# Kernel optimization log

Measured on AMD Instinct MI355X. Metric: run time of the kernel, lower is better.

## Reference

```python
import jax, jax.numpy as jnp
import numpy as np

ALPHA = 1.0      # focal_alpha
GAMMA = 2.0      # focal_gamma
MARGIN = 0.3     # triplet_margin
T = 3.0          # kd_temperature
FW, TW, KW = 1.0, 0.5, 1.0  # focal/triplet/kd weights
NEG_INF_FILL = 1000000.0


def setup_inputs() -> dict:
    key = jax.random.key(0)
    k1, k2, k3, k4 = jax.random.split(key, 4)
    B, D, C = 4096, 512, 2
    return {
        "logits": jax.random.normal(k1, (B, C), jnp.float32),
        "features": jax.random.normal(k2, (B, D), jnp.float32),
        "hard_labels": jax.random.randint(k3, (B,), 0, 2),
        "soft_labels": jax.random.uniform(k4, (B, C), jnp.float32),
    }


def _pairwise_dist(x):
    # torch.cdist(x, x, p=2): [B, B] euclidean distances, safe sqrt (grad-safe at 0)
    sq = jnp.sum(x * x, axis=1)
    d2 = jnp.maximum(sq[:, None] + sq[None, :] - 2.0 * (x @ x.T), 0.0)
    safe = jnp.where(d2 > 0, d2, 1.0)
    return jnp.where(d2 > 0, jnp.sqrt(safe), 0.0)


def reference(logits, features, hard_labels, soft_labels):
    B = logits.shape[0]
    # ---- focal loss (integer-label branch) ----
    logp = jax.nn.log_softmax(logits, axis=-1)
    ce = -jnp.take_along_axis(logp, hard_labels[:, None], axis=1)[:, 0]
    pt = jnp.exp(-ce)
    focal = jnp.mean(ALPHA * (1.0 - pt) ** GAMMA * ce)

    # ---- triplet loss: batch-hard mining, vectorized over rows ----
    d = _pairwise_dist(features)                      # [B, B]
    same = hard_labels[:, None] == hard_labels[None, :]
    eye = jnp.eye(B, dtype=bool)
    mpos = (same & ~eye).astype(d.dtype)              # positives, diag zeroed
    mneg = (~same).astype(d.dtype)                    # negatives
    posd = d * mpos
    valid = (jnp.sum(posd, axis=1) > 0).astype(d.dtype)
    hardest_pos = jnp.max(posd, axis=1)
    hardest_neg = jnp.min(d * mneg + (1.0 - mneg) * NEG_INF_FILL, axis=1)
    per_row = jax.nn.relu(hardest_pos - hardest_neg + MARGIN)
    n_valid = jnp.sum(valid)
    triplet = jnp.where(n_valid > 0,
                        jnp.sum(per_row * valid) / jnp.maximum(n_valid, 1.0),
                        0.0)

    # ---- KD loss: KLDiv(batchmean) * T^2 ----
    student_log = jax.nn.log_softmax(logits / T, axis=-1)
    teacher = jax.nn.softmax(jnp.log(soft_labels + 1e-8) / T, axis=-1)
    kd = jnp.sum(teacher * (jnp.log(teacher) - student_log)) / B * (T ** 2)

    total = FW * focal + TW * triplet + KW * kd
    return total, focal, triplet, kd
```

## Files before the change

### kernel.cpp

```cpp
#include <hip/hip_runtime.h>
#include <hip/hip_bf16.h>

#define B_ROWS 4096
#define D_FEAT 512

typedef short s16x8 __attribute__((ext_vector_type(8)));
typedef float f32x4 __attribute__((ext_vector_type(4)));

#define GLOAD_LDS16(gsrc, ldst)                                                        \
    __builtin_amdgcn_global_load_lds(                                                  \
        (const __attribute__((address_space(1))) void*)(gsrc),                         \
        (__attribute__((address_space(3))) void*)(ldst), 16, 0, 0)

__device__ inline float waveReduceSum(float v) {
#pragma unroll
    for (int off = 32; off > 0; off >>= 1) v += __shfl_xor(v, off);
    return v;
}

__global__ __launch_bounds__(256) void prep_kernel(const float* __restrict__ feat,
                                                   const float* __restrict__ logits,
                                                   const int* __restrict__ labels,
                                                   const float* __restrict__ soft,
                                                   short* __restrict__ featbf,
                                                   float* __restrict__ sqn,
                                                   unsigned* __restrict__ posmax,
                                                   float* __restrict__ negminf,
                                                   float* __restrict__ fpart,
                                                   float* __restrict__ kpart) {
    const int bid = blockIdx.x, tid = threadIdx.x;
    const int wave = tid >> 6, lane = tid & 63;
    const int row = bid * 4 + wave;

    const float* p = feat + (size_t)row * D_FEAT + lane * 8;
    float4 a = *(const float4*)p;
    float4 b = *(const float4*)(p + 4);
    float vals[8] = {a.x, a.y, a.z, a.w, b.x, b.y, b.z, b.w};
    short outv[8];
    float s = 0.f;
#pragma unroll
    for (int j = 0; j < 8; ++j) {
        __hip_bfloat16 h = __float2bfloat16(vals[j]);
        outv[j] = *(short*)&h;
        float xb = __bfloat162float(h);
        s = fmaf(xb, xb, s);
    }
    *(s16x8*)(featbf + (size_t)row * D_FEAT + lane * 8) = *(s16x8*)outv;
    s = waveReduceSum(s);
    if (lane == 0) sqn[row] = s;

    if (tid < 4) posmax[bid * 4 + tid] = 0u;
    else if (tid < 8) negminf[bid * 4 + tid - 4] = 1e12f;

    if (bid < 16) {
        int i = bid * 256 + tid;
        float l0 = logits[2 * i], l1 = logits[2 * i + 1];

        float m = fmaxf(l0, l1);
        float lse = m + logf(expf(l0 - m) + expf(l1 - m));
        float lp = (labels[i] ? l1 : l0) - lse;
        float ce = -lp;
        float pt = expf(lp);
        float om = 1.f - pt;
        float focal = om * om * ce;

        const float Tinv = 1.f / 3.f;
        float s0 = l0 * Tinv, s1 = l1 * Tinv;
        float ms = fmaxf(s0, s1);
        float lses = ms + logf(expf(s0 - ms) + expf(s1 - ms));
        float sl0 = s0 - lses, sl1 = s1 - lses;
        float t0 = logf(soft[2 * i] + 1e-8f) * Tinv;
        float t1 = logf(soft[2 * i + 1] + 1e-8f) * Tinv;
        float mt = fmaxf(t0, t1);
        float lset = mt + logf(expf(t0 - mt) + expf(t1 - mt));
        float tl0 = t0 - lset, tl1 = t1 - lset;
        float p0 = expf(tl0), p1 = expf(tl1);
        float kd = p0 * (tl0 - sl0) + p1 * (tl1 - sl1);

        float fs = waveReduceSum(focal);
        float ks = waveReduceSum(kd);
        __shared__ float sf[4], sk[4];
        if (lane == 0) { sf[wave] = fs; sk[wave] = ks; }
        __syncthreads();
        if (tid == 0) {
            fpart[bid] = sf[0] + sf[1] + sf[2] + sf[3];
            kpart[bid] = sk[0] + sk[1] + sk[2] + sk[3];
        }
    }
}

__global__ __launch_bounds__(512) void pairwise_256_kernel(const short* __restrict__ featbf,
                                                           const float* __restrict__ sqn,
                                                           const int* __restrict__ labels,
                                                           unsigned* __restrict__ posmax,
                                                           unsigned* __restrict__ negmin) {
    __shared__ short As0[256 * 64], As1[256 * 64];
    __shared__ short Bs0[256 * 64], Bs1[256 * 64];
    const int tid = threadIdx.x;
    const int bfl = blockIdx.x;
    const int xcd = bfl & 7, loc = bfl >> 3;
    const int ib = (xcd & 3) * 4 + (loc & 3);
    const int jb = (xcd >> 1 & 2) * 4 + (loc >> 2);
    const int wid = tid >> 6, lane = tid & 63;
    const int wr = wid >> 2, wc = wid & 3;
    const int lo = lane & 15, hi = lane >> 4;

    const short* Asrc[4];
    const short* Bsrc[4];
    int dstoff[4];
#pragma unroll
    for (int q = 0; q < 4; ++q) {
        int row = q * 64 + wid * 8 + (lane >> 3);
        int c = (lane & 7) ^ (row & 7);
        Asrc[q] = featbf + (size_t)(ib * 256 + row) * D_FEAT + c * 8;
        Bsrc[q] = featbf + (size_t)(jb * 256 + row) * D_FEAT + c * 8;
        dstoff[q] = (q * 64 + wid * 8) * 64;
    }

    int aoff[2][8], boff[2][4];
#pragma unroll
    for (int ks = 0; ks < 2; ++ks) {
#pragma unroll
        for (int m = 0; m < 8; ++m) {
            int ar = wr * 128 + m * 16 + lo;
            aoff[ks][m] = ar * 64 + ((ks * 4 + hi) ^ (ar & 7)) * 8;
        }
#pragma unroll
        for (int n = 0; n < 4; ++n) {
            int bc = wc * 64 + n * 16 + lo;
            boff[ks][n] = bc * 64 + ((ks * 4 + hi) ^ (bc & 7)) * 8;
        }
    }

    f32x4 acc[8][4];
#pragma unroll
    for (int m = 0; m < 8; ++m)
#pragma unroll
        for (int n = 0; n < 4; ++n)
            acc[m][n] = (f32x4){0.f, 0.f, 0.f, 0.f};

#define STAGE_TILE(Adst, Bdst, kkv)                                                    \
    {                                                                                  \
        _Pragma("unroll") for (int q = 0; q < 4; ++q) {                                \
            GLOAD_LDS16(Asrc[q] + (kkv) * 64, (Adst) + dstoff[q]);                     \
            GLOAD_LDS16(Bsrc[q] + (kkv) * 64, (Bdst) + dstoff[q]);                     \
        }                                                                              \
    }

#define COMPUTE_TILE(Abuf, Bbuf)                                                       \
    {                                                                                  \
        _Pragma("unroll") for (int ks = 0; ks < 2; ++ks) {                             \
            s16x8 af[8], bfr[4];                                                       \
            _Pragma("unroll") for (int m = 0; m < 8; ++m)                              \
                af[m] = *(const s16x8*)((Abuf) + aoff[ks][m]);                         \
            _Pragma("unroll") for (int n = 0; n < 4; ++n)                              \
                bfr[n] = *(const s16x8*)((Bbuf) + boff[ks][n]);                        \
            _Pragma("unroll") for (int m = 0; m < 8; ++m)                              \
                _Pragma("unroll") for (int n = 0; n < 4; ++n)                          \
                    acc[m][n] = __builtin_amdgcn_mfma_f32_16x16x32_bf16(               \
                        af[m], bfr[n], acc[m][n], 0, 0, 0);                            \
        }                                                                              \
    }

    short *Aa = As0, *Ab = As1, *Ba = Bs0, *Bb = Bs1;
    STAGE_TILE(Aa, Ba, 0);
    asm volatile("s_waitcnt vmcnt(0)" ::: "memory");
    __builtin_amdgcn_s_barrier();
    __builtin_amdgcn_sched_barrier(0);

    for (int kk = 0; kk < D_FEAT / 64 - 1; ++kk) {
        STAGE_TILE(Ab, Bb, kk + 1);
        COMPUTE_TILE(Aa, Ba);
        asm volatile("s_waitcnt vmcnt(0)" ::: "memory");
        __builtin_amdgcn_s_barrier();
        __builtin_amdgcn_sched_barrier(0);
        short* t;
        t = Aa; Aa = Ab; Ab = t;
        t = Ba; Ba = Bb; Bb = t;
    }
    COMPUTE_TILE(Aa, Ba);

#undef STAGE_TILE
#undef COMPUTE_TILE

    int coln[4], labc[4];
    float sqc[4];
#pragma unroll
    for (int n = 0; n < 4; ++n) {
        coln[n] = jb * 256 + wc * 64 + n * 16 + lo;
        labc[n] = labels[coln[n]];
        sqc[n] = sqn[coln[n]];
    }
    __syncthreads();
    float (*redp)[5] = (float(*)[5])As0;
    float (*redn)[5] = ((float(*)[5])As0) + 256;

#pragma unroll
    for (int m = 0; m < 8; ++m) {
#pragma unroll
        for (int r = 0; r < 4; ++r) {
            int row_loc = wr * 128 + m * 16 + hi * 4 + r;
            int row_g = ib * 256 + row_loc;
            int labr = labels[row_g];
            float sqr = sqn[row_g];
            float pm = 0.f, nm = 1e12f;
#pragma unroll
            for (int n = 0; n < 4; ++n) {
                float d2 = fmaxf(sqr + fmaf(-2.f, acc[m][n][r], sqc[n]), 0.f);
                bool same = (labr == labc[n]);
                if (same) {
                    if (row_g != coln[n]) pm = fmaxf(pm, d2);
                } else {
                    nm = fminf(nm, d2);
                }
            }
#pragma unroll
            for (int off = 1; off < 16; off <<= 1) {
                pm = fmaxf(pm, __shfl_xor(pm, off));
                nm = fminf(nm, __shfl_xor(nm, off));
            }
            if (lo == 0) {
                redp[row_loc][wc] = pm;
                redn[row_loc][wc] = nm;
            }
        }
    }
    __syncthreads();
    if (tid < 256) {
        float p = fmaxf(fmaxf(redp[tid][0], redp[tid][1]),
                        fmaxf(redp[tid][2], redp[tid][3]));
        atomicMax(&posmax[ib * 256 + tid], __float_as_uint(p));
    } else {
        int row = tid - 256;
        float nn = fminf(fminf(redn[row][0], redn[row][1]),
                         fminf(redn[row][2], redn[row][3]));
        atomicMin(&negmin[ib * 256 + row], __float_as_uint(nn));
    }
}

__global__ __launch_bounds__(256) void finalize_kernel(const unsigned* __restrict__ posmax,
                                                       const unsigned* __restrict__ negmin,
                                                       const float* __restrict__ fpart,
                                                       const float* __restrict__ kpart,
                                                       float* __restrict__ out) {
    int tid = threadIdx.x;
    float sum_pr = 0.f, sum_v = 0.f;
    for (int i = tid; i < B_ROWS; i += 256) {
        float p2 = __uint_as_float(posmax[i]);
        float n2 = __uint_as_float(negmin[i]);
        float v = (p2 > 0.f) ? 1.f : 0.f;
        sum_pr += fmaxf(sqrtf(p2) - sqrtf(n2) + 0.3f, 0.f) * v;
        sum_v += v;
    }
    sum_pr = waveReduceSum(sum_pr);
    sum_v = waveReduceSum(sum_v);
    __shared__ float sp[4], sv[4];
    int wave = tid >> 6, lane = tid & 63;
    if (lane == 0) { sp[wave] = sum_pr; sv[wave] = sum_v; }
    __syncthreads();
    if (tid == 0) {
        float spr = sp[0] + sp[1] + sp[2] + sp[3];
        float svv = sv[0] + sv[1] + sv[2] + sv[3];
        float fsum = 0.f, ksum = 0.f;
        for (int b = 0; b < 16; ++b) { fsum += fpart[b]; ksum += kpart[b]; }
        float focal = fsum / 4096.f;
        float kd = ksum / 4096.f * 9.f;
        float triplet = (svv > 0.f) ? spr / fmaxf(svv, 1.f) : 0.f;
        float total = focal + 0.5f * triplet + kd;
        out[0] = total;
        out[1] = focal;
        out[2] = triplet;
        out[3] = kd;
    }
}

extern "C" void kernel_launch(void* const* d_in, const int* in_sizes, int n_in,
                              void* d_out, int out_size, void* d_ws, size_t ws_size,
                              hipStream_t stream) {
    const float* logits = (const float*)d_in[0];
    const float* feat   = (const float*)d_in[1];
    const int*   labels = (const int*)d_in[2];
    const float* soft   = (const float*)d_in[3];

    char* ws = (char*)d_ws;
    unsigned* posmax = (unsigned*)ws;
    unsigned* negmin = (unsigned*)(ws + 16384);
    float*    sqn    = (float*)(ws + 32768);
    float*    fpart  = (float*)(ws + 49152);
    float*    kpart  = (float*)(ws + 49152 + 256);
    short*    featbf = (short*)(ws + 65536);

    prep_kernel<<<1024, 256, 0, stream>>>(feat, logits, labels, soft, featbf, sqn,
                                          posmax, (float*)negmin, fpart, kpart);
    pairwise_256_kernel<<<256, 512, 0, stream>>>(featbf, sqn, labels, posmax, negmin);
    finalize_kernel<<<1, 256, 0, stream>>>(posmax, negmin, fpart, kpart,
                                           (float*)d_out);
}
```

Baseline: 46.03 us.

## Split pairwise GEMM K-loop into eight interleaved load/compute phases

Restructures the bf16 MFMA main loop of the pairwise-distance kernel into four phases per K tile (two M halves times two K sub-steps). Each phase issues part of the next tile's global-to-LDS loads, waits with fine-grained vmcnt counts and uses s_setprio around its MFMA block. LDS is re-laid out as 32-element K halves with a new XOR swizzle. The goal is to overlap memory traffic with matrix math instead of waiting on a full vmcnt(0) barrier every tile. In exchange it adds twice as many barriers per tile and depends on getting the hand-counted vmcnt values exactly right.

```diff
diff --git a/kernel.cpp b/kernel.cpp
--- a/kernel.cpp
+++ b/kernel.cpp
@@ -89,7 +89,7 @@
     }
 }
 
-__global__ __launch_bounds__(512) void pairwise_256_kernel(const short* __restrict__ featbf,
+__global__ __launch_bounds__(512) void pairwise_8ph_kernel(const short* __restrict__ featbf,
                                                            const float* __restrict__ sqn,
                                                            const int* __restrict__ labels,
                                                            unsigned* __restrict__ posmax,
@@ -100,36 +100,37 @@
     const int bfl = blockIdx.x;
     const int xcd = bfl & 7, loc = bfl >> 3;
     const int ib = (xcd & 3) * 4 + (loc & 3);
-    const int jb = (xcd >> 1 & 2) * 4 + (loc >> 2);
+    const int jb = ((xcd >> 1) & 2) * 4 + (loc >> 2);
     const int wid = tid >> 6, lane = tid & 63;
     const int wr = wid >> 2, wc = wid & 3;
     const int lo = lane & 15, hi = lane >> 4;
 
-    const short* Asrc[4];
-    const short* Bsrc[4];
-    int dstoff[4];
-#pragma unroll
-    for (int q = 0; q < 4; ++q) {
-        int row = q * 64 + wid * 8 + (lane >> 3);
-        int c = (lane & 7) ^ (row & 7);
-        Asrc[q] = featbf + (size_t)(ib * 256 + row) * D_FEAT + c * 8;
-        Bsrc[q] = featbf + (size_t)(jb * 256 + row) * D_FEAT + c * 8;
-        dstoff[q] = (q * 64 + wid * 8) * 64;
-    }
-
-    int aoff[2][8], boff[2][4];
-#pragma unroll
-    for (int ks = 0; ks < 2; ++ks) {
-#pragma unroll
-        for (int m = 0; m < 8; ++m) {
-            int ar = wr * 128 + m * 16 + lo;
-            aoff[ks][m] = ar * 64 + ((ks * 4 + hi) ^ (ar & 7)) * 8;
-        }
-#pragma unroll
-        for (int n = 0; n < 4; ++n) {
-            int bc = wc * 64 + n * 16 + lo;
-            boff[ks][n] = bc * 64 + ((ks * 4 + hi) ^ (bc & 7)) * 8;
-        }
+    const int rbA0 = (wid < 4) ? wid * 16 : 64 + wid * 16;
+    const int rbB0 = wid * 16;
+    const int rA0 = rbA0 + (lane >> 2), rA1 = rA0 + 64;
+    const int rB0 = rbB0 + (lane >> 2), rB1 = rB0 + 128;
+    const int cA0 = (lane & 3) ^ ((rA0 >> 1) & 3), cA1 = (lane & 3) ^ ((rA1 >> 1) & 3);
+    const int cB0 = (lane & 3) ^ ((rB0 >> 1) & 3), cB1 = (lane & 3) ^ ((rB1 >> 1) & 3);
+    const short* gA0 = featbf + (size_t)(ib * 256 + rA0) * D_FEAT + cA0 * 8;
+    const short* gA1 = featbf + (size_t)(ib * 256 + rA1) * D_FEAT + cA1 * 8;
+    const short* gB0 = featbf + (size_t)(jb * 256 + rB0) * D_FEAT + cB0 * 8;
+    const short* gB1 = featbf + (size_t)(jb * 256 + rB1) * D_FEAT + cB1 * 8;
+    const int dA0 = rbA0 * 32, dA1 = (rbA0 + 64) * 32;
+    const int dB0 = rbB0 * 32, dB1 = (rbB0 + 128) * 32;
+
+#define ISSUE(gptr, buf, dstbase, ksv, ktv)                                            \
+    GLOAD_LDS16((gptr) + (ktv) * 64 + (ksv) * 32, (buf) + (ksv) * 8192 + (dstbase))
+
+    int aoffs[8], boffs[4];
+#pragma unroll
+    for (int m = 0; m < 8; ++m) {
+        int r = wr * 128 + m * 16 + lo;
+        aoffs[m] = r * 32 + ((hi ^ ((r >> 1) & 3)) * 8);
+    }
+#pragma unroll
+    for (int n = 0; n < 4; ++n) {
+        int r = wc * 64 + n * 16 + lo;
+        boffs[n] = r * 32 + ((hi ^ ((r >> 1) & 3)) * 8);
     }
 
     f32x4 acc[8][4];
@@ -139,49 +140,77 @@
         for (int n = 0; n < 4; ++n)
             acc[m][n] = (f32x4){0.f, 0.f, 0.f, 0.f};
 
-#define STAGE_TILE(Adst, Bdst, kkv)                                                    \
+#define PHASE(mh, ksv, DO_BFR, ISSUES, VMCNT)                                          \
     {                                                                                  \
-        _Pragma("unroll") for (int q = 0; q < 4; ++q) {                                \
-            GLOAD_LDS16(Asrc[q] + (kkv) * 64, (Adst) + dstoff[q]);                     \
-            GLOAD_LDS16(Bsrc[q] + (kkv) * 64, (Bdst) + dstoff[q]);                     \
+        if (DO_BFR) {                                                                  \
+            _Pragma("unroll") for (int n = 0; n < 4; ++n)                              \
+                bfr[n] = *(const s16x8*)(Bcur + (ksv) * 8192 + boffs[n]);              \
         }                                                                              \
-    }
-
-#define COMPUTE_TILE(Abuf, Bbuf)                                                       \
-    {                                                                                  \
-        _Pragma("unroll") for (int ks = 0; ks < 2; ++ks) {                             \
-            s16x8 af[8], bfr[4];                                                       \
-            _Pragma("unroll") for (int m = 0; m < 8; ++m)                              \
-                af[m] = *(const s16x8*)((Abuf) + aoff[ks][m]);                         \
+        s16x8 af[4];                                                                   \
+        _Pragma("unroll") for (int mi = 0; mi < 4; ++mi)                               \
+            af[mi] = *(const s16x8*)(Acur + (ksv) * 8192 + aoffs[(mh) * 4 + mi]);      \
+        ISSUES;                                                                        \
+        __builtin_amdgcn_s_barrier();                                                  \
+        __builtin_amdgcn_sched_barrier(0);                                             \
+        __builtin_amdgcn_s_setprio(1);                                                 \
+        _Pragma("unroll") for (int mi = 0; mi < 4; ++mi)                               \
             _Pragma("unroll") for (int n = 0; n < 4; ++n)                              \
-                bfr[n] = *(const s16x8*)((Bbuf) + boff[ks][n]);                        \
-            _Pragma("unroll") for (int m = 0; m < 8; ++m)                              \
-                _Pragma("unroll") for (int n = 0; n < 4; ++n)                          \
-                    acc[m][n] = __builtin_amdgcn_mfma_f32_16x16x32_bf16(               \
-                        af[m], bfr[n], acc[m][n], 0, 0, 0);                            \
-        }                                                                              \
-    }
-
-    short *Aa = As0, *Ab = As1, *Ba = Bs0, *Bb = Bs1;
-    STAGE_TILE(Aa, Ba, 0);
-    asm volatile("s_waitcnt vmcnt(0)" ::: "memory");
+                acc[(mh) * 4 + mi][n] = __builtin_amdgcn_mfma_f32_16x16x32_bf16(       \
+                    af[mi], bfr[n], acc[(mh) * 4 + mi][n], 0, 0, 0);                   \
+        __builtin_amdgcn_s_setprio(0);                                                 \
+        VMCNT;                                                                         \
+        __builtin_amdgcn_s_barrier();                                                  \
+        __builtin_amdgcn_sched_barrier(0);                                             \
+    }
+
+#define VM(n) asm volatile("s_waitcnt vmcnt(" #n ")" ::: "memory")
+
+    const short* Acur = As0;
+    const short* Bcur = Bs0;
+    short* Anxt = As1;
+    short* Bnxt = Bs1;
+
+    ISSUE(gA0, As0, dA0, 0, 0);
+    ISSUE(gB0, Bs0, dB0, 0, 0);
+    ISSUE(gB1, Bs0, dB1, 0, 0);
+    ISSUE(gA1, As0, dA1, 0, 0);
+    ISSUE(gA0, As0, dA0, 1, 0);
+    ISSUE(gB0, Bs0, dB0, 1, 0);
+    ISSUE(gB1, Bs0, dB1, 1, 0);
+    ISSUE(gA1, As0, dA1, 1, 0);
+    VM(5);
     __builtin_amdgcn_s_barrier();
     __builtin_amdgcn_sched_barrier(0);
 
-    for (int kk = 0; kk < D_FEAT / 64 - 1; ++kk) {
-        STAGE_TILE(Ab, Bb, kk + 1);
-        COMPUTE_TILE(Aa, Ba);
-        asm volatile("s_waitcnt vmcnt(0)" ::: "memory");
-        __builtin_amdgcn_s_barrier();
-        __builtin_amdgcn_sched_barrier(0);
-        short* t;
-        t = Aa; Aa = Ab; Ab = t;
-        t = Ba; Ba = Bb; Bb = t;
-    }
-    COMPUTE_TILE(Aa, Ba);
-
-#undef STAGE_TILE
-#undef COMPUTE_TILE
+#pragma unroll 1
+    for (int kt = 0; kt < D_FEAT / 64 - 1; ++kt) {
+        s16x8 bfr[4];
+        PHASE(0, 0, true,
+              { ISSUE(gA0, Anxt, dA0, 0, kt + 1); ISSUE(gB0, Bnxt, dB0, 0, kt + 1); },
+              VM(6));
+        PHASE(1, 0, false,
+              { ISSUE(gB1, Bnxt, dB1, 0, kt + 1); ISSUE(gA1, Anxt, dA1, 0, kt + 1); },
+              VM(5));
+        PHASE(0, 1, true,
+              { ISSUE(gA0, Anxt, dA0, 1, kt + 1); ISSUE(gB0, Bnxt, dB0, 1, kt + 1); },
+              VM(6));
+        PHASE(1, 1, false,
+              { ISSUE(gB1, Bnxt, dB1, 1, kt + 1); ISSUE(gA1, Anxt, dA1, 1, kt + 1); },
+              VM(5));
+        const short* t1 = Acur; Acur = Anxt; Anxt = (short*)t1;
+        const short* t2 = Bcur; Bcur = Bnxt; Bnxt = (short*)t2;
+    }
+    {
+        s16x8 bfr[4];
+        PHASE(0, 0, true,  {}, VM(4));
+        PHASE(1, 0, false, {}, VM(1));
+        PHASE(0, 1, true,  {}, VM(0));
+        PHASE(1, 1, false, {}, {});
+    }
+
+#undef PHASE
+#undef VM
+#undef ISSUE
 
     int coln[4], labc[4];
     float sqc[4];
@@ -292,7 +321,7 @@
 
     prep_kernel<<<1024, 256, 0, stream>>>(feat, logits, labels, soft, featbf, sqn,
                                           posmax, (float*)negmin, fpart, kpart);
-    pairwise_256_kernel<<<256, 512, 0, stream>>>(featbf, sqn, labels, posmax, negmin);
+    pairwise_8ph_kernel<<<256, 512, 0, stream>>>(featbf, sqn, labels, posmax, negmin);
     finalize_kernel<<<1, 256, 0, stream>>>(posmax, negmin, fpart, kpart,
                                            (float*)d_out);
 }
```

New measurement: 44.23 us. 1.04x faster.
